# Optimization experiments

Measured on AMD Instinct MI355X. Metric: run time of the kernel, lower is better.

The kernel has to match this reference:

```python
import jax, jax.numpy as jnp
import numpy as np

B, S, DIM = 4, 2048, 1024
HEADS, HD = 16, DIM // 16
HIDDEN, LEVELS = 4 * DIM, 3
LN_EPS = 1e-5


def setup_inputs() -> dict:
    key = jax.random.key(0)
    ks = jax.random.split(key, 10)
    w = lambda k, shape: (jax.random.normal(k, shape, jnp.float32) * 0.02)
    return {
        "x": jax.random.normal(ks[0], (B, S, DIM), jnp.float32),
        "Wq": w(ks[1], (DIM, DIM)),
        "Wk": w(ks[2], (DIM, DIM)),
        "Wv": w(ks[3], (DIM, DIM)),
        "Wo": w(ks[4], (DIM, DIM)),
        "ln1_g": jnp.ones((DIM,), jnp.float32),
        "ln1_b": jnp.zeros((DIM,), jnp.float32),
        "ln2_g": jnp.ones((DIM,), jnp.float32),
        "ln2_b": jnp.zeros((DIM,), jnp.float32),
        "cms_w1": w(ks[5], (LEVELS, DIM, HIDDEN)),
        "cms_b1": jnp.zeros((LEVELS, HIDDEN), jnp.float32),
        "cms_w2": w(ks[6], (LEVELS, HIDDEN, DIM)),
        "cms_b2": jnp.zeros((LEVELS, DIM), jnp.float32),
    }


def _layer_norm(x, g, b):
    m = jnp.mean(x, axis=-1, keepdims=True)
    v = jnp.var(x, axis=-1, keepdims=True)
    return (x - m) * jax.lax.rsqrt(v + LN_EPS) * g + b


def _linear_attn(h, Wq, Wk, Wv, Wo):
    # h: [B, S, DIM]; feature_map(z) = elu(z) + 1 applied to Q and K
    fm = lambda z: jax.nn.elu(z) + 1.0
    Q = fm(h @ Wq).reshape(B, S, HEADS, HD)
    K = fm(h @ Wk).reshape(B, S, HEADS, HD)
    V = (h @ Wv).reshape(B, S, HEADS, HD)
    # scan over time with fast-weight memory M_t = M_{t-1} + k_t (x) v_t
    Qs = jnp.moveaxis(Q, 1, 0)  # [S, B, H, D]
    Ks = jnp.moveaxis(K, 1, 0)
    Vs = jnp.moveaxis(V, 1, 0)

    def step(carry, qkv):
        mem, ksum = carry  # [B,H,D,D], [B,H,D]
        q, k, v = qkv      # each [B,H,D]
        mem = mem + k[..., :, None] * v[..., None, :]
        ksum = ksum + k
        num = jnp.einsum('bhde,bhd->bhe', mem, q)
        den = jnp.einsum('bhd,bhd->bh', ksum, q)[..., None] + 1e-6
        return (mem, ksum), num / den

    init = (jnp.zeros((B, HEADS, HD, HD), h.dtype),
            jnp.zeros((B, HEADS, HD), h.dtype))
    _, ys = jax.lax.scan(step, init, (Qs, Ks, Vs))  # ys: [S,B,H,D]
    out = jnp.moveaxis(ys, 0, 1).reshape(B, S, DIM)
    return out @ Wo


def _cms(h, w1, b1, w2, b2):
    # Continuum Memory System: chain of LEVELS MLPs (dim->4dim->dim).
    y = h
    for l in range(LEVELS):
        y = jax.nn.gelu(y @ w1[l] + b1[l]) @ w2[l] + b2[l]
    return y


def reference(x, Wq, Wk, Wv, Wo, ln1_g, ln1_b, ln2_g, ln2_b,
              cms_w1, cms_b1, cms_w2, cms_b2):
    x = x + _linear_attn(_layer_norm(x, ln1_g, ln1_b), Wq, Wk, Wv, Wo)
    x = x + _cms(_layer_norm(x, ln2_g, ln2_b), cms_w1, cms_b1, cms_w2, cms_b2)
    return x
```

## Files before the change

### kernel.cpp

```cpp
#include <hip/hip_runtime.h>
#include <stdint.h>
#include <math.h>

#define DIM     1024
#define HID     4096
#define SEQ     2048
#define NB      4
#define NH      16
#define HD      64
#define NCHUNK  32
#define MROWS   8192
#define QSTR    3072

typedef unsigned short ushort_t;
typedef __attribute__((ext_vector_type(8))) short bf16x8;
typedef __attribute__((ext_vector_type(4))) float f32x4;

#define OFF_H    ((size_t)0)
#define OFF_Q    ((size_t)16777216)
#define OFF_P    ((size_t)67108864)
#define OFF_KS   ((size_t)100663296)
#define OFF_X1   ((size_t)101187584)
#define OFF_WQT  ((size_t)134742016)
#define OFF_WOT  ((size_t)141033472)
#define OFF_W1T  ((size_t)143130624)
#define OFF_W2T  ((size_t)168296448)
#define OFF_HIDB OFF_Q + 16777216

__device__ __forceinline__ float b2f(ushort_t u) {
    return __uint_as_float(((unsigned int)u) << 16);
}
__device__ __forceinline__ ushort_t f2b(float f) {
    unsigned int u = __float_as_uint(f);
    u += 0x7FFFu + ((u >> 16) & 1u);
    return (ushort_t)(u >> 16);
}
__device__ __forceinline__ void unpack4(uint2 u, float* f) {
    f[0] = __uint_as_float(u.x << 16);
    f[1] = __uint_as_float(u.x & 0xffff0000u);
    f[2] = __uint_as_float(u.y << 16);
    f[3] = __uint_as_float(u.y & 0xffff0000u);
}
__device__ __forceinline__ float fast_gelu(float x) {
    const float u = x * (1.5957691216057308f + 0.07135481627f * x * x);
    const float e = exp2f(-1.4426950408889634f * u);
    return x * __builtin_amdgcn_rcpf(1.0f + e);
}
__device__ __forceinline__ float fast_elu1(float x) {
    return x > 0.0f ? x + 1.0f : exp2f(1.4426950408889634f * x);
}
__device__ __forceinline__ void ldg16(const ushort_t* g, ushort_t* l) {
    __builtin_amdgcn_global_load_lds(
        (const __attribute__((address_space(1))) void*)g,
        (__attribute__((address_space(3))) void*)l, 16, 0, 0);
}

__global__ void __launch_bounds__(256)
transpose_f32_bf16(const float* __restrict__ src, ushort_t* __restrict__ dst, int R, int C)
{
    __shared__ float t[32][33];
    const int bx = blockIdx.x * 32;
    const int by = blockIdx.y * 32;
    const int tx = threadIdx.x, ty = threadIdx.y;
    #pragma unroll
    for (int i = ty; i < 32; i += 8)
        t[i][tx] = src[(size_t)(by + i) * C + bx + tx];
    __syncthreads();
    #pragma unroll
    for (int i = ty; i < 32; i += 8)
        dst[(size_t)(bx + i) * R + by + tx] = f2b(t[tx][i]);
}

__global__ void __launch_bounds__(256)
ln_fwd(const float* __restrict__ xin, const float* __restrict__ g,
       const float* __restrict__ be, ushort_t* __restrict__ out)
{
    const int row = blockIdx.x, tid = threadIdx.x;
    const float4 f = ((const float4*)(xin + (size_t)row * DIM))[tid];
    float v[4] = {f.x, f.y, f.z, f.w};
    float s  = v[0] + v[1] + v[2] + v[3];
    float ss = v[0]*v[0] + v[1]*v[1] + v[2]*v[2] + v[3]*v[3];
    #pragma unroll
    for (int off = 32; off; off >>= 1) {
        s  += __shfl_down(s, off);
        ss += __shfl_down(ss, off);
    }
    __shared__ float red[2][4];
    const int wave = tid >> 6, lane = tid & 63;
    if (lane == 0) { red[0][wave] = s; red[1][wave] = ss; }
    __syncthreads();
    s  = red[0][0] + red[0][1] + red[0][2] + red[0][3];
    ss = red[1][0] + red[1][1] + red[1][2] + red[1][3];
    const float mean = s * (1.0f / DIM);
    const float var  = ss * (1.0f / DIM) - mean * mean;
    const float rstd = rsqrtf(var + 1e-5f);
    ushort_t o[4];
    #pragma unroll
    for (int i = 0; i < 4; i++) {
        const int col = tid * 4 + i;
        o[i] = f2b((v[i] - mean) * rstd * g[col] + be[col]);
    }
    uint2 u2;
    u2.x = (unsigned int)o[0] | ((unsigned int)o[1] << 16);
    u2.y = (unsigned int)o[2] | ((unsigned int)o[3] << 16);
    *(uint2*)(out + (size_t)row * DIM + tid * 4) = u2;
}

#define ACT_NONE 0
#define ACT_ELU1 1
#define ACT_GELU 2
#define ACT_QKV  3


#define G256_RD_A(BUF, FR0) \
    _Pragma("unroll") for (int _i = 0; _i < 4; ++_i) \
    _Pragma("unroll") for (int _kk = 0; _kk < 2; ++_kk) \
        af[_i][_kk] = *(const bf16x8*)(ldsb + (BUF) + aoff + (((FR0) + _i) << 11) \
                                       + (((_kk << 6) | qv16) ^ mflip))

#define G256_RD_B(BUF, FC0, CNT) \
    _Pragma("unroll") for (int _c = 0; _c < (CNT); ++_c) \
    _Pragma("unroll") for (int _kk = 0; _kk < 2; ++_kk) \
        bf[(FC0) + _c][_kk] = *(const bf16x8*)(ldsb + (BUF) + boff + (((FC0) + _c) << 11) \
                                               + (((_kk << 6) | qv16) ^ mflip))

#define G256_MFMA(AR, C0, CNT) \
    _Pragma("unroll") for (int _i = 0; _i < 4; ++_i) \
    _Pragma("unroll") for (int _c = 0; _c < (CNT); ++_c) \
    _Pragma("unroll") for (int _kk = 0; _kk < 2; ++_kk) \
        acc[(AR) + _i][(C0) + _c] = __builtin_amdgcn_mfma_f32_16x16x32_bf16( \
            af[_i][_kk], bf[(C0) + _c][_kk], acc[(AR) + _i][(C0) + _c], 0, 0, 0)

#define G256_STAGE_A(T, H) do { \
    char* _d = ldsb + (((T) & 1) ? (int)BUFSZ : 0) + ((H) << 14) + (tid << 4); \
    const ushort_t* _s = pA + (size_t)((H) * 128) * K + (size_t)(T) * 64; \
    ldg16(_s, (ushort_t*)_d); \
    ldg16(_s + (size_t)64 * K, (ushort_t*)(_d + 8192)); \
} while (0)

#define G256_STAGE_B(T, H) do { \
    char* _d = ldsb + (((T) & 1) ? (int)BUFSZ : 0) + 32768 + (H) * (BN_ * 64) + (tid << 4); \
    const ushort_t* _s = pB + (size_t)((H) * (BN_ >> 1)) * K + (size_t)(T) * 64; \
    ldg16(_s, (ushort_t*)_d); \
    if (BN_ == 256) ldg16(_s + (size_t)64 * K, (ushort_t*)(_d + 8192)); \
} while (0)

#define G256_BARW() do { \
    __builtin_amdgcn_s_barrier(); \
    asm volatile("s_waitcnt lgkmcnt(0)" ::: "memory"); \
    __builtin_amdgcn_sched_barrier(0); \
    __builtin_amdgcn_s_setprio(1); \
} while (0)

#define G256_ENDP() do { \
    __builtin_amdgcn_s_setprio(0); \
    __builtin_amdgcn_s_barrier(); \
} while (0)

template<int BN_, int ACT, bool BIAS, bool RES, bool OUTF32>
__global__ void __launch_bounds__(512, 2)
gemm256(const ushort_t* __restrict__ A, const ushort_t* __restrict__ Bt,
        const float* __restrict__ bias, const float* __restrict__ resid,
        void* __restrict__ Cout, int M, int N, int K)
{
    constexpr int NF    = BN_ / 64;
    constexpr int BUFSZ = 32768 + BN_ * 128;
    __shared__ __align__(16) char ldsb[2 * BUFSZ];

    const int tid  = threadIdx.x;
    const int lane = tid & 63, wave = tid >> 6;
    const int wm_idx = wave >> 2, wn_idx = wave & 3;
    const int bm = blockIdx.x * 256, bn = blockIdx.y * BN_;

    const int r0  = tid >> 3;
    const int kbs = (((tid & 7) ^ (r0 & 7)) << 4);
    const ushort_t* pA = A  + (size_t)(bm + r0) * K + (kbs >> 1);
    const ushort_t* pB = Bt + (size_t)(bn + r0) * K + (kbs >> 1);

    const int m     = lane & 15;
    const int qv16  = (lane >> 4) << 4;
    const int mflip = (m & 7) << 4;
    const int aoff  = (wm_idx * 128 + m) << 7;
    const int boff  = 32768 + ((wn_idx * (BN_ >> 2) + m) << 7);

    f32x4  acc[8][NF] = {};
    bf16x8 af[4][2], bf[NF][2];

    const int NT    = K >> 6;
    const int niter = NT >> 1;

    G256_STAGE_A(0, 0); G256_STAGE_A(0, 1);
    G256_STAGE_B(0, 0); G256_STAGE_B(0, 1);
    G256_STAGE_A(1, 0);
    asm volatile("s_waitcnt vmcnt(2)" ::: "memory");
    __builtin_amdgcn_s_barrier();

    for (int it = 0; it < niter; ++it) {
        const int  t    = it << 1;
        const bool more = (it + 1) < niter;

        G256_RD_A(0, 0); G256_RD_B(0, 0, NF / 2);
        G256_STAGE_A(t + 1, 1);
        G256_BARW(); G256_MFMA(0, 0, NF / 2); G256_ENDP();

        G256_RD_B(0, NF / 2, NF / 2);
        G256_STAGE_B(t + 1, 0);
        G256_BARW(); G256_MFMA(0, NF / 2, NF / 2); G256_ENDP();

        G256_RD_A(0, 4);
        G256_STAGE_B(t + 1, 1);
        G256_BARW(); G256_MFMA(4, 0, NF / 2); G256_ENDP();

        if (more) G256_STAGE_A(t + 2, 0);
        G256_BARW(); G256_MFMA(4, NF / 2, NF / 2);
        __builtin_amdgcn_s_setprio(0);
        if (more) asm volatile("s_waitcnt vmcnt(2)" ::: "memory");
        else      asm volatile("s_waitcnt vmcnt(0)" ::: "memory");
        __builtin_amdgcn_s_barrier();

        G256_RD_A(BUFSZ, 0); G256_RD_B(BUFSZ, 0, NF / 2);
        if (more) G256_STAGE_A(t + 2, 1);
        G256_BARW(); G256_MFMA(0, 0, NF / 2); G256_ENDP();

        G256_RD_B(BUFSZ, NF / 2, NF / 2);
        if (more) G256_STAGE_B(t + 2, 0);
        G256_BARW(); G256_MFMA(0, NF / 2, NF / 2); G256_ENDP();

        G256_RD_A(BUFSZ, 4);
        if (more) G256_STAGE_B(t + 2, 1);
        G256_BARW(); G256_MFMA(4, 0, NF / 2); G256_ENDP();

        if (more) G256_STAGE_A(t + 3, 0);
        G256_BARW(); G256_MFMA(4, NF / 2, NF / 2);
        __builtin_amdgcn_s_setprio(0);
        if (more) asm volatile("s_waitcnt vmcnt(2)" ::: "memory");
        else      asm volatile("s_waitcnt vmcnt(0)" ::: "memory");
        __builtin_amdgcn_s_barrier();
    }

    const int cr   = (lane >> 4) << 2;
    const int ccol = lane & 15;
    #pragma unroll
    for (int fr = 0; fr < 8; ++fr) {
        #pragma unroll
        for (int fc = 0; fc < NF; ++fc) {
            const int gc = bn + wn_idx * (BN_ >> 2) + fc * 16 + ccol;
            const float bv = BIAS ? bias[gc] : 0.0f;
            #pragma unroll
            for (int j = 0; j < 4; ++j) {
                const int gr = bm + wm_idx * 128 + fr * 16 + cr + j;
                float vv = acc[fr][fc][j] + bv;
                if (ACT == ACT_ELU1) vv = fast_elu1(vv);
                if (ACT == ACT_GELU) vv = fast_gelu(vv);
                if (ACT == ACT_QKV)  vv = (bn < 2048) ? fast_elu1(vv) : vv;
                const size_t oidx = (size_t)gr * N + gc;
                if (RES) vv += resid[oidx];
                if (OUTF32) ((float*)Cout)[oidx] = vv;
                else        ((ushort_t*)Cout)[oidx] = f2b(vv);
            }
        }
    }
    (void)M;
}

__global__ void __launch_bounds__(256)
attn_phase1(const ushort_t* __restrict__ qkv,
            float* __restrict__ P, float* __restrict__ Ksum)
{
    const int c = blockIdx.x, h = blockIdx.y, b = blockIdx.z;
    __shared__ ushort_t Ks[64][68], Vs[64][68];
    const int tid = threadIdx.x;
    const size_t rowbase = (size_t)b * SEQ + c * 64;
    #pragma unroll
    for (int i = 0; i < 4; i++) {
        const int lin = tid + 256 * i;
        const int t = lin >> 4, d4 = (lin & 15) * 4;
        const size_t gidx = (rowbase + t) * QSTR + h * HD + d4;
        *(uint2*)&Ks[t][d4] = *(const uint2*)(qkv + 1024 + gidx);
        *(uint2*)&Vs[t][d4] = *(const uint2*)(qkv + 2048 + gidx);
    }
    __syncthreads();
    const int d0 = (tid >> 4) * 4, e0 = (tid & 15) * 4;
    float acc[4][4] = {};
    for (int t = 0; t < 64; t++) {
        float kf[4], vf[4];
        unpack4(*(const uint2*)&Ks[t][d0], kf);
        unpack4(*(const uint2*)&Vs[t][e0], vf);
        #pragma unroll
        for (int i = 0; i < 4; i++)
            #pragma unroll
            for (int j = 0; j < 4; j++)
                acc[i][j] += kf[i] * vf[j];
    }
    const size_t pbase = (((size_t)b * NH + h) * NCHUNK + c) * 4096;
    #pragma unroll
    for (int i = 0; i < 4; i++) {
        float4 o; o.x = acc[i][0]; o.y = acc[i][1]; o.z = acc[i][2]; o.w = acc[i][3];
        *(float4*)(P + pbase + (size_t)(d0 + i) * 64 + e0) = o;
    }
    if (tid < 64) {
        float a = 0.0f;
        for (int t = 0; t < 64; t++) a += b2f(Ks[t][tid]);
        Ksum[(((size_t)b * NH + h) * NCHUNK + c) * 64 + tid] = a;
    }
}

__global__ void __launch_bounds__(256)
attn_prefix(float* __restrict__ P, float* __restrict__ Ksum)
{
    const int bh = blockIdx.y;
    const int e  = blockIdx.x * 256 + threadIdx.x;
    const size_t base = (size_t)bh * NCHUNK * 4096 + e;
    float acc = 0.0f;
    #pragma unroll
    for (int c = 0; c < NCHUNK; c++) {
        const float t = P[base + (size_t)c * 4096];
        P[base + (size_t)c * 4096] = acc;
        acc += t;
    }
    if (blockIdx.x == 0 && threadIdx.x < 64) {
        const size_t kb = (size_t)bh * NCHUNK * 64 + threadIdx.x;
        float a = 0.0f;
        #pragma unroll
        for (int c = 0; c < NCHUNK; c++) {
            const float t = Ksum[kb + c * 64];
            Ksum[kb + c * 64] = a;
            a += t;
        }
    }
}

__global__ void __launch_bounds__(256)
attn_phase2(const ushort_t* __restrict__ qkv, const float* __restrict__ P,
            const float* __restrict__ Ksum, ushort_t* __restrict__ Out)
{
    const int c = blockIdx.x, h = blockIdx.y, b = blockIdx.z;
    const int tid = threadIdx.x;
    __shared__ ushort_t Qs[64][68], KsB[64][68], VsB[64][68];
    __shared__ float S[64][68];
    __shared__ float Mp[64][64];
    __shared__ float kp[64];
    __shared__ float partial[4][64];
    const size_t rowbase = (size_t)b * SEQ + c * 64;
    const size_t pbase = (((size_t)b * NH + h) * NCHUNK + c) * 4096;
    #pragma unroll
    for (int i = 0; i < 4; i++) {
        const int lin = tid + 256 * i;
        const int t = lin >> 4, d4 = (lin & 15) * 4;
        const size_t gidx = (rowbase + t) * QSTR + h * HD + d4;
        *(uint2*)&Qs[t][d4]  = *(const uint2*)(qkv + gidx);
        *(uint2*)&KsB[t][d4] = *(const uint2*)(qkv + 1024 + gidx);
        *(uint2*)&VsB[t][d4] = *(const uint2*)(qkv + 2048 + gidx);
        *(float4*)&Mp[t][d4] = *(const float4*)(P + pbase + lin * 4);
    }
    if (tid < 64) kp[tid] = Ksum[(((size_t)b * NH + h) * NCHUNK + c) * 64 + tid];
    __syncthreads();

    const int t0 = (tid >> 4) * 4;
    const int c0 = (tid & 15) * 4;

    {
        float accS[4][4] = {};
        for (int d4 = 0; d4 < 64; d4 += 4) {
            float qf[4][4], kf[4][4];
            #pragma unroll
            for (int i = 0; i < 4; i++) {
                unpack4(*(const uint2*)&Qs[t0 + i][d4], qf[i]);
                unpack4(*(const uint2*)&KsB[c0 + i][d4], kf[i]);
            }
            #pragma unroll
            for (int i = 0; i < 4; i++)
                #pragma unroll
                for (int j = 0; j < 4; j++)
                    #pragma unroll
                    for (int dd = 0; dd < 4; dd++)
                        accS[i][j] += qf[i][dd] * kf[j][dd];
        }
        #pragma unroll
        for (int i = 0; i < 4; i++) {
            float4 sv;
            sv.x = (c0 + 0 <= t0 + i) ? accS[i][0] : 0.0f;
            sv.y = (c0 + 1 <= t0 + i) ? accS[i][1] : 0.0f;
            sv.z = (c0 + 2 <= t0 + i) ? accS[i][2] : 0.0f;
            sv.w = (c0 + 3 <= t0 + i) ? accS[i][3] : 0.0f;
            *(float4*)&S[t0 + i][c0] = sv;
        }
    }
    __syncthreads();

    {
        const int t = tid & 63, q = tid >> 6;
        const int base = q * 16;
        float a = 0.0f;
        #pragma unroll
        for (int ii = 0; ii < 16; ii++) a += S[t][base + ii];
        #pragma unroll
        for (int d = 0; d < 16; d++) a += b2f(Qs[t][base + d]) * kp[base + d];
        partial[q][t] = a;
    }
    __syncthreads();

    float acc[4][4] = {};
    for (int ii = 0; ii < 64; ii++) {
        float vf[4];
        unpack4(*(const uint2*)&VsB[ii][c0], vf);
        #pragma unroll
        for (int i = 0; i < 4; i++) {
            const float s = S[t0 + i][ii];
            #pragma unroll
            for (int j = 0; j < 4; j++) acc[i][j] += s * vf[j];
        }
    }
    for (int d = 0; d < 64; d++) {
        const float4 mp = *(const float4*)&Mp[d][c0];
        #pragma unroll
        for (int i = 0; i < 4; i++) {
            const float qv = b2f(Qs[t0 + i][d]);
            acc[i][0] += qv * mp.x; acc[i][1] += qv * mp.y;
            acc[i][2] += qv * mp.z; acc[i][3] += qv * mp.w;
        }
    }
    #pragma unroll
    for (int i = 0; i < 4; i++) {
        const float dent = partial[0][t0 + i] + partial[1][t0 + i] +
                           partial[2][t0 + i] + partial[3][t0 + i] + 1e-6f;
        const float r = 1.0f / dent;
        ushort_t o[4];
        #pragma unroll
        for (int j = 0; j < 4; j++) o[j] = f2b(acc[i][j] * r);
        uint2 u2;
        u2.x = (unsigned int)o[0] | ((unsigned int)o[1] << 16);
        u2.y = (unsigned int)o[2] | ((unsigned int)o[3] << 16);
        *(uint2*)(Out + (rowbase + t0 + i) * DIM + h * HD + c0) = u2;
    }
}

extern "C" void kernel_launch(void* const* d_in, const int* in_sizes, int n_in,
                              void* d_out, int out_size, void* d_ws, size_t ws_size,
                              hipStream_t stream)
{
    const float* x      = (const float*)d_in[0];
    const float* Wq     = (const float*)d_in[1];
    const float* Wk     = (const float*)d_in[2];
    const float* Wv     = (const float*)d_in[3];
    const float* Wo     = (const float*)d_in[4];
    const float* ln1g   = (const float*)d_in[5];
    const float* ln1b   = (const float*)d_in[6];
    const float* ln2g   = (const float*)d_in[7];
    const float* ln2b   = (const float*)d_in[8];
    const float* cw1    = (const float*)d_in[9];
    const float* cb1    = (const float*)d_in[10];
    const float* cw2    = (const float*)d_in[11];
    const float* cb2    = (const float*)d_in[12];

    char* ws = (char*)d_ws;
    ushort_t* h     = (ushort_t*)(ws + OFF_H);
    ushort_t* qkv   = (ushort_t*)(ws + OFF_Q);
    float*    Pb    = (float*)(ws + OFF_P);
    float*    ksb   = (float*)(ws + OFF_KS);
    float*    x1    = (float*)(ws + OFF_X1);
    ushort_t* wqkvt = (ushort_t*)(ws + OFF_WQT);
    ushort_t* wot   = (ushort_t*)(ws + OFF_WOT);
    ushort_t* w1t   = (ushort_t*)(ws + OFF_W1T);
    ushort_t* w2t   = (ushort_t*)(ws + OFF_W2T);
    ushort_t* hid   = (ushort_t*)(ws + OFF_HIDB);
    float*    outp  = (float*)d_out;

    const dim3 tb(32, 8);
    transpose_f32_bf16<<<dim3(32, 32), tb, 0, stream>>>(Wq, wqkvt,                   DIM, DIM);
    transpose_f32_bf16<<<dim3(32, 32), tb, 0, stream>>>(Wk, wqkvt + 1024 * 1024,     DIM, DIM);
    transpose_f32_bf16<<<dim3(32, 32), tb, 0, stream>>>(Wv, wqkvt + 2 * 1024 * 1024, DIM, DIM);
    transpose_f32_bf16<<<dim3(32, 32), tb, 0, stream>>>(Wo, wot, DIM, DIM);
    for (int l = 0; l < 3; l++) {
        transpose_f32_bf16<<<dim3(128, 32), tb, 0, stream>>>(cw1 + (size_t)l * DIM * HID,
                                                             w1t + (size_t)l * HID * DIM, DIM, HID);
        transpose_f32_bf16<<<dim3(32, 128), tb, 0, stream>>>(cw2 + (size_t)l * HID * DIM,
                                                             w2t + (size_t)l * DIM * HID, HID, DIM);
    }

    ln_fwd<<<MROWS, 256, 0, stream>>>(x, ln1g, ln1b, h);

    gemm256<128, ACT_QKV, false, false, false><<<dim3(32, 24), 512, 0, stream>>>(
        h, wqkvt, nullptr, nullptr, qkv, MROWS, QSTR, DIM);

    attn_phase1<<<dim3(NCHUNK, NH, NB), 256, 0, stream>>>(qkv, Pb, ksb);
    attn_prefix<<<dim3(16, 64), 256, 0, stream>>>(Pb, ksb);
    attn_phase2<<<dim3(NCHUNK, NH, NB), 256, 0, stream>>>(qkv, Pb, ksb, h);

    gemm256<128, ACT_NONE, false, true, true><<<dim3(32, 8), 512, 0, stream>>>(
        h, wot, nullptr, x, x1, MROWS, DIM, DIM);

    ln_fwd<<<MROWS, 256, 0, stream>>>(x1, ln2g, ln2b, h);

    const ushort_t* cur = h;
    for (int l = 0; l < 3; l++) {
        gemm256<256, ACT_GELU, true, false, false><<<dim3(32, 16), 512, 0, stream>>>(
            cur, w1t + (size_t)l * HID * DIM, cb1 + (size_t)l * HID, nullptr, hid, MROWS, HID, DIM);
        if (l < 2) {
            gemm256<128, ACT_NONE, true, false, false><<<dim3(32, 8), 512, 0, stream>>>(
                hid, w2t + (size_t)l * DIM * HID, cb2 + (size_t)l * DIM, nullptr, h, MROWS, DIM, HID);
            cur = h;
        } else {
            gemm256<128, ACT_NONE, true, true, true><<<dim3(32, 8), 512, 0, stream>>>(
                hid, w2t + (size_t)l * DIM * HID, cb2 + (size_t)l * DIM, x1, outp, MROWS, DIM, HID);
        }
    }
    (void)in_sizes; (void)n_in; (void)out_size; (void)ws_size;
}
```

Before: 848.9 us.

## Restructure GEMM pipeline to prefetch two tiles ahead and interleave B columns

Reworks the 256-row GEMM main loop so each LDS buffer is refilled with the tile two steps ahead once its own MFMAs have read it, instead of staging the next tile into the other buffer mid-computation. The prologue now loads both buffers up front and waits with a deeper vmcnt, keeping more global loads in flight. B fragments are remapped so each wave takes interleaved 16-column groups strided by 64, and the epilogue column index is changed to match. This deepens latency hiding but changes the LDS write/read ordering against the barriers, which risks hazards and puts more loads in flight per thread.

```diff
diff --git a/kernel.cpp b/kernel.cpp
--- a/kernel.cpp
+++ b/kernel.cpp
@@ -112,48 +112,63 @@
 #define ACT_QKV  3
 
 
-#define G256_RD_A(BUF, FR0) \
+#define G_RD_A(BUF, FR0) \
     _Pragma("unroll") for (int _i = 0; _i < 4; ++_i) \
     _Pragma("unroll") for (int _kk = 0; _kk < 2; ++_kk) \
         af[_i][_kk] = *(const bf16x8*)(ldsb + (BUF) + aoff + (((FR0) + _i) << 11) \
                                        + (((_kk << 6) | qv16) ^ mflip))
 
-#define G256_RD_B(BUF, FC0, CNT) \
-    _Pragma("unroll") for (int _c = 0; _c < (CNT); ++_c) \
+#define G_RD_B(BUF, F) \
     _Pragma("unroll") for (int _kk = 0; _kk < 2; ++_kk) \
-        bf[(FC0) + _c][_kk] = *(const bf16x8*)(ldsb + (BUF) + boff + (((FC0) + _c) << 11) \
-                                               + (((_kk << 6) | qv16) ^ mflip))
-
-#define G256_MFMA(AR, C0, CNT) \
+        bf[(F)][_kk] = *(const bf16x8*)(ldsb + (BUF) + boff + ((F) << 13) \
+                                        + (((_kk << 6) | qv16) ^ mflip))
+
+#define G_MFMA(AR, C0, CNT) \
     _Pragma("unroll") for (int _i = 0; _i < 4; ++_i) \
     _Pragma("unroll") for (int _c = 0; _c < (CNT); ++_c) \
     _Pragma("unroll") for (int _kk = 0; _kk < 2; ++_kk) \
         acc[(AR) + _i][(C0) + _c] = __builtin_amdgcn_mfma_f32_16x16x32_bf16( \
             af[_i][_kk], bf[(C0) + _c][_kk], acc[(AR) + _i][(C0) + _c], 0, 0, 0)
 
-#define G256_STAGE_A(T, H) do { \
-    char* _d = ldsb + (((T) & 1) ? (int)BUFSZ : 0) + ((H) << 14) + (tid << 4); \
-    const ushort_t* _s = pA + (size_t)((H) * 128) * K + (size_t)(T) * 64; \
-    ldg16(_s, (ushort_t*)_d); \
-    ldg16(_s + (size_t)64 * K, (ushort_t*)(_d + 8192)); \
-} while (0)
-
-#define G256_STAGE_B(T, H) do { \
-    char* _d = ldsb + (((T) & 1) ? (int)BUFSZ : 0) + 32768 + (H) * (BN_ * 64) + (tid << 4); \
-    const ushort_t* _s = pB + (size_t)((H) * (BN_ >> 1)) * K + (size_t)(T) * 64; \
-    ldg16(_s, (ushort_t*)_d); \
-    if (BN_ == 256) ldg16(_s + (size_t)64 * K, (ushort_t*)(_d + 8192)); \
-} while (0)
-
-#define G256_BARW() do { \
+#define ST_A(BUFO, T, R) ldg16(pA + (size_t)(R) * K + (size_t)(T) * 64, \
+    (ushort_t*)(ldsb + (BUFO) + ((R) << 7) + (tid << 4)))
+#define ST_B(BUFO, T, R) ldg16(pB + (size_t)(R) * K + (size_t)(T) * 64, \
+    (ushort_t*)(ldsb + (BUFO) + 32768 + ((R) << 7) + (tid << 4)))
+
+#define G_BARW() do { \
     __builtin_amdgcn_s_barrier(); \
     asm volatile("s_waitcnt lgkmcnt(0)" ::: "memory"); \
     __builtin_amdgcn_sched_barrier(0); \
     __builtin_amdgcn_s_setprio(1); \
 } while (0)
 
-#define G256_ENDP() do { \
+#define G_ENDP() do { \
     __builtin_amdgcn_s_setprio(0); \
+    __builtin_amdgcn_s_barrier(); \
+} while (0)
+
+#define G_TILE(BUFO, TS) do { \
+     \
+    G_RD_A(BUFO, 0); \
+    _Pragma("unroll") for (int _f = 0; _f < NF / 2; ++_f) G_RD_B(BUFO, _f); \
+    G_BARW(); G_MFMA(0, 0, NF / 2); G_ENDP(); \
+     \
+    _Pragma("unroll") for (int _f = NF / 2; _f < NF; ++_f) G_RD_B(BUFO, _f); \
+    if (more) { ST_A(BUFO, TS, 0); ST_A(BUFO, TS, 128); ST_B(BUFO, TS, 0); } \
+    G_BARW(); G_MFMA(0, NF / 2, NF / 2); G_ENDP(); \
+     \
+    G_RD_A(BUFO, 4); \
+    if (more) { \
+        ST_B(BUFO, TS, 64); \
+        if constexpr (NF == 4) { ST_B(BUFO, TS, 128); ST_B(BUFO, TS, 192); } \
+    } \
+    G_BARW(); G_MFMA(4, 0, NF / 2); G_ENDP(); \
+     \
+    if (more) { ST_A(BUFO, TS, 64); ST_A(BUFO, TS, 192); } \
+    G_BARW(); G_MFMA(4, NF / 2, NF / 2); \
+    __builtin_amdgcn_s_setprio(0); \
+    if (more) asm volatile("s_waitcnt vmcnt(%0)" :: "i"(LPT) : "memory"); \
+    else      asm volatile("s_waitcnt vmcnt(0)" ::: "memory"); \
     __builtin_amdgcn_s_barrier(); \
 } while (0)
 
@@ -165,6 +180,7 @@
 {
     constexpr int NF    = BN_ / 64;
     constexpr int BUFSZ = 32768 + BN_ * 128;
+    constexpr int LPT   = 4 + NF;
     __shared__ __align__(16) char ldsb[2 * BUFSZ];
 
     const int tid  = threadIdx.x;
@@ -181,7 +197,7 @@
     const int qv16  = (lane >> 4) << 4;
     const int mflip = (m & 7) << 4;
     const int aoff  = (wm_idx * 128 + m) << 7;
-    const int boff  = 32768 + ((wn_idx * (BN_ >> 2) + m) << 7);
+    const int boff  = 32768 + ((wn_idx * 16 + m) << 7);
 
     f32x4  acc[8][NF] = {};
     bf16x8 af[4][2], bf[NF][2];
@@ -189,53 +205,20 @@
     const int NT    = K >> 6;
     const int niter = NT >> 1;
 
-    G256_STAGE_A(0, 0); G256_STAGE_A(0, 1);
-    G256_STAGE_B(0, 0); G256_STAGE_B(0, 1);
-    G256_STAGE_A(1, 0);
-    asm volatile("s_waitcnt vmcnt(2)" ::: "memory");
+    ST_A(0, 0, 0); ST_A(0, 0, 64); ST_A(0, 0, 128); ST_A(0, 0, 192);
+    ST_B(0, 0, 0); ST_B(0, 0, 64);
+    if constexpr (NF == 4) { ST_B(0, 0, 128); ST_B(0, 0, 192); }
+    ST_A(BUFSZ, 1, 0); ST_A(BUFSZ, 1, 64); ST_A(BUFSZ, 1, 128); ST_A(BUFSZ, 1, 192);
+    ST_B(BUFSZ, 1, 0); ST_B(BUFSZ, 1, 64);
+    if constexpr (NF == 4) { ST_B(BUFSZ, 1, 128); ST_B(BUFSZ, 1, 192); }
+    asm volatile("s_waitcnt vmcnt(%0)" :: "i"(LPT) : "memory");
     __builtin_amdgcn_s_barrier();
 
     for (int it = 0; it < niter; ++it) {
         const int  t    = it << 1;
         const bool more = (it + 1) < niter;
-
-        G256_RD_A(0, 0); G256_RD_B(0, 0, NF / 2);
-        G256_STAGE_A(t + 1, 1);
-        G256_BARW(); G256_MFMA(0, 0, NF / 2); G256_ENDP();
-
-        G256_RD_B(0, NF / 2, NF / 2);
-        G256_STAGE_B(t + 1, 0);
-        G256_BARW(); G256_MFMA(0, NF / 2, NF / 2); G256_ENDP();
-
-        G256_RD_A(0, 4);
-        G256_STAGE_B(t + 1, 1);
-        G256_BARW(); G256_MFMA(4, 0, NF / 2); G256_ENDP();
-
-        if (more) G256_STAGE_A(t + 2, 0);
-        G256_BARW(); G256_MFMA(4, NF / 2, NF / 2);
-        __builtin_amdgcn_s_setprio(0);
-        if (more) asm volatile("s_waitcnt vmcnt(2)" ::: "memory");
-        else      asm volatile("s_waitcnt vmcnt(0)" ::: "memory");
-        __builtin_amdgcn_s_barrier();
-
-        G256_RD_A(BUFSZ, 0); G256_RD_B(BUFSZ, 0, NF / 2);
-        if (more) G256_STAGE_A(t + 2, 1);
-        G256_BARW(); G256_MFMA(0, 0, NF / 2); G256_ENDP();
-
-        G256_RD_B(BUFSZ, NF / 2, NF / 2);
-        if (more) G256_STAGE_B(t + 2, 0);
-        G256_BARW(); G256_MFMA(0, NF / 2, NF / 2); G256_ENDP();
-
-        G256_RD_A(BUFSZ, 4);
-        if (more) G256_STAGE_B(t + 2, 1);
-        G256_BARW(); G256_MFMA(4, 0, NF / 2); G256_ENDP();
-
-        if (more) G256_STAGE_A(t + 3, 0);
-        G256_BARW(); G256_MFMA(4, NF / 2, NF / 2);
-        __builtin_amdgcn_s_setprio(0);
-        if (more) asm volatile("s_waitcnt vmcnt(2)" ::: "memory");
-        else      asm volatile("s_waitcnt vmcnt(0)" ::: "memory");
-        __builtin_amdgcn_s_barrier();
+        G_TILE(0,     t + 2);
+        G_TILE(BUFSZ, t + 3);
     }
 
     const int cr   = (lane >> 4) << 2;
@@ -244,7 +227,7 @@
     for (int fr = 0; fr < 8; ++fr) {
         #pragma unroll
         for (int fc = 0; fc < NF; ++fc) {
-            const int gc = bn + wn_idx * (BN_ >> 2) + fc * 16 + ccol;
+            const int gc = bn + fc * 64 + wn_idx * 16 + ccol;
             const float bv = BIAS ? bias[gc] : 0.0f;
             #pragma unroll
             for (int j = 0; j < 4; ++j) {
```

Result: slower. 892.5 us (+5.1%).
